# Kernel optimization log

Hardware: AMD Instinct MI355X
Metric: run time of the kernel (lower is better)

## Reference

```python
import jax, jax.numpy as jnp
import numpy as np
from jax import lax

B, N, C = 8, 16384, 4
NUM_GROUPS = 128
GROUP_SIZE = 32
GROUP_RADIUS = 0.1
UPSCALE_K = 128
OVERLAP_FACTOR = 0.7


def setup_inputs() -> dict:
    key = jax.random.key(0)
    k1, k2 = jax.random.split(key)
    # xyz in [0,1]^3, energy in [0,1] at channel 3
    points = jax.random.uniform(k1, (B, N, C), dtype=jnp.float32)
    lengths = jax.random.randint(k2, (B,), N // 2, N + 1).astype(jnp.int32)
    return {"points": points, "lengths": lengths}


def _fps(xyz, lengths, K):
    """Farthest point sampling. xyz: (B,N,3) -> centers (B,K,3), idx (B,K)."""
    B_, N_, _ = xyz.shape
    valid = jnp.arange(N_)[None, :] < lengths[:, None]          # (B,N)
    mind0 = jnp.where(valid, jnp.inf, -jnp.inf)                 # running min dist
    start = jnp.zeros((B_,), jnp.int32)                         # fixed start point
    batch = jnp.arange(B_)

    def step(carry, _):
        mind, cur = carry
        c = xyz[batch, cur]                                     # (B,3)
        d = jnp.sum((xyz - c[:, None, :]) ** 2, axis=-1)        # (B,N)
        mind = jnp.minimum(mind, jnp.where(valid, d, -jnp.inf))
        nxt = jnp.argmax(mind, axis=1).astype(jnp.int32)
        return (mind, nxt), cur

    _, idxs = lax.scan(step, (mind0, start), None, length=K)
    idxs = idxs.T                                               # (B,K)
    centers = xyz[batch[:, None], idxs]                         # (B,K,3)
    return centers, idxs


def _cnms(centers, radius, overlap_factor):
    """Greedy cluster-NMS over FPS-ordered centers. Returns keep mask (B,G)."""
    B_, G, _ = centers.shape
    d2 = jnp.sum((centers[:, :, None, :] - centers[:, None, :, :]) ** 2, axis=-1)
    thr = (2.0 * radius * (1.0 - overlap_factor)) ** 2          # spheres overlap > factor

    def step(keep, j):
        conflict = jnp.any(keep & (d2[:, j, :] < thr), axis=-1)
        keep = keep.at[:, j].set(~conflict)
        return keep, None

    keep, _ = lax.scan(step, jnp.zeros((B_, G), bool), jnp.arange(G))
    return keep


def _ball_query(centers, xyz, lengths, retain, K, radius):
    """First-K points within radius of each center (pytorch3d semantics); -1 pad."""
    N_ = xyz.shape[1]
    d2 = jnp.sum((centers[:, :, None, :] - xyz[:, None, :, :]) ** 2, axis=-1)  # (B,G,N)
    in_len = (jnp.arange(N_)[None, :] < lengths[:, None])[:, None, :]
    valid = (d2 <= radius * radius) & in_len & retain[:, :, None]
    # pick the K smallest point indices among valid ones -> "first K found"
    key_ = jnp.where(valid, jnp.arange(N_, dtype=jnp.int32)[None, None, :], N_)
    negv, _ = lax.top_k(-key_, K)                               # (B,G,K)
    idx = -negv
    return jnp.where(idx == N_, -1, idx)


def reference(points, lengths):
    xyz = points[..., :3]
    centers, _ = _fps(xyz, lengths, NUM_GROUPS)                 # (B,G,3)
    retain = _cnms(centers, GROUP_RADIUS, OVERLAP_FACTOR)       # (B,G)
    idx = _ball_query(centers, xyz, lengths, retain, UPSCALE_K, GROUP_RADIUS)

    # select_topk_by_energy (energies_idx = 3)
    batch = jnp.arange(points.shape[0])[:, None, None]
    invalid = idx == -1
    energies = jnp.where(invalid, -jnp.inf, points[batch, jnp.clip(idx, 0), 3])
    topv, topi = lax.top_k(energies, GROUP_SIZE)                # (B,G,K_new)
    tidx = jnp.take_along_axis(idx, topi, axis=2)
    tidx = jnp.where(jnp.isneginf(topv), -1, tidx)

    # fill_empty_indices: replace -1 with the group's first index
    fidx = jnp.where(tidx == -1, tidx[:, :, :1], tidx)

    # masked_gather: -1 -> gather 0 then zero out
    groups = points[batch, jnp.clip(fidx, 0)]                   # (B,G,K,C)
    groups = jnp.where((fidx == -1)[..., None], 0.0, groups)

    group_lengths = jnp.sum(jnp.all(tidx != -1, axis=2), axis=1)  # (B,)
    embedding_mask = jnp.arange(NUM_GROUPS)[None, :] < group_lengths[:, None]

    # center xyz channels, then scale ALL channels by radius (as in source)
    groups = groups.at[..., :3].add(-centers[:, :, None, :])
    groups = groups / GROUP_RADIUS
    return groups, centers, embedding_mask
```

## Files before the change

kernel.cpp:

```cpp
#include <hip/hip_runtime.h>
#include <math.h>

#define B_ 8
#define N_ 16384
#define G_ 128
#define GS_ 32
#define UK_ 128
#define FPS_T 512
#define FPS_W 8
#define PPT 32
#define BQ_T 512
#define BQ_W 8

#pragma clang fp contract(off)

typedef float v2f __attribute__((ext_vector_type(2)));

#define DPP64_MAXSTEP(vv, ctrl, rmask)                                          \
  {                                                                             \
    unsigned _lo = (unsigned)__builtin_amdgcn_update_dpp(                       \
        0, (int)(unsigned)((vv) & 0xffffffffull), (ctrl), (rmask), 0xf, false); \
    unsigned _hi = (unsigned)__builtin_amdgcn_update_dpp(                       \
        0, (int)(unsigned)((vv) >> 32), (ctrl), (rmask), 0xf, false);           \
    unsigned long long _tv = ((unsigned long long)_hi << 32) | _lo;             \
    if (_tv > (vv)) (vv) = _tv;                                                 \
  }

__device__ __forceinline__ float dist2(float x, float y, float z,
                                       float cx, float cy, float cz) {
    float dx = __fsub_rn(x, cx);
    float dy = __fsub_rn(y, cy);
    float dz = __fsub_rn(z, cz);
    return __fadd_rn(__fadd_rn(__fmul_rn(dx, dx), __fmul_rn(dy, dy)),
                     __fmul_rn(dz, dz));
}

__global__ void init_kernel(int* __restrict__ gl) {
    int t = threadIdx.x;
    if (t < B_) gl[t] = 0;
}

__global__ __launch_bounds__(FPS_T, 2) void fps_cnms_kernel(
    const float4* __restrict__ pts, const int* __restrict__ lengths,
    float* __restrict__ centers_out, int* __restrict__ keep_out) {
    const int b = blockIdx.x;
    const int t = threadIdx.x;
    const int lane = t & 63;
    const int wv = t >> 6;
    const int len = lengths[b];
    const float4* p = pts + (size_t)b * N_;

    __shared__ __align__(16) unsigned long long s_part[2][FPS_W];
    __shared__ float s_cen[G_][3];

    v2f xp[PPT / 2], yp[PPT / 2], zp[PPT / 2];
    v2f mp[PPT / 2];
#pragma unroll
    for (int j = 0; j < PPT / 2; j += 2) {
        int nA0 = (2 * j) * FPS_T + t;
        float4 qA0, qB0, qA1, qB1;
        const float4* a0 = p + nA0;
        const float4* b0 = a0 + FPS_T;
        const float4* a1 = a0 + 2 * FPS_T;
        const float4* b1 = a0 + 3 * FPS_T;
        asm volatile(
            "global_load_dwordx4 %0, %4, off\n\t"
            "global_load_dwordx4 %1, %5, off\n\t"
            "global_load_dwordx4 %2, %6, off\n\t"
            "global_load_dwordx4 %3, %7, off\n\t"
            "s_waitcnt vmcnt(0)"
            : "=&v"(qA0), "=&v"(qB0), "=&v"(qA1), "=&v"(qB1)
            : "v"(a0), "v"(b0), "v"(a1), "v"(b1)
            : "memory");
        xp[j]     = (v2f){qA0.x, qB0.x};
        yp[j]     = (v2f){qA0.y, qB0.y};
        zp[j]     = (v2f){qA0.z, qB0.z};
        xp[j + 1] = (v2f){qA1.x, qB1.x};
        yp[j + 1] = (v2f){qA1.y, qB1.y};
        zp[j + 1] = (v2f){qA1.z, qB1.z};
        v2f mm0, mm1;
        mm0.x = (nA0 < len)             ? INFINITY : -INFINITY;
        mm0.y = (nA0 + FPS_T < len)     ? INFINITY : -INFINITY;
        mm1.x = (nA0 + 2 * FPS_T < len) ? INFINITY : -INFINITY;
        mm1.y = (nA0 + 3 * FPS_T < len) ? INFINITY : -INFINITY;
        mp[j] = mm0;
        mp[j + 1] = mm1;
    }

    int n = 0;
    for (int k = 0; k < G_; k++) {
        float4 c = p[n];
        if (t == 0) {
            centers_out[(b * G_ + k) * 3 + 0] = c.x;
            centers_out[(b * G_ + k) * 3 + 1] = c.y;
            centers_out[(b * G_ + k) * 3 + 2] = c.z;
            s_cen[k][0] = c.x; s_cen[k][1] = c.y; s_cen[k][2] = c.z;
        }
        if (k == G_ - 1) break;

        v2f cXX = {c.x, c.x};
        v2f cYY = {c.y, c.y};
        v2f cZZ = {c.z, c.z};

#pragma unroll
        for (int j = 0; j < PPT / 2; j++) {
            v2f dx = xp[j] - cXX;
            v2f dy = yp[j] - cYY;
            v2f dz = zp[j] - cZZ;
            v2f dd = (dx * dx + dy * dy) + dz * dz;
            mp[j] = __builtin_elementwise_min(mp[j], dd);
        }

        v2f t8[8];
#pragma unroll
        for (int j = 0; j < 8; j++)
            t8[j] = __builtin_elementwise_max(mp[2 * j], mp[2 * j + 1]);
        v2f t4a = __builtin_elementwise_max(t8[0], t8[1]);
        v2f t4b = __builtin_elementwise_max(t8[2], t8[3]);
        v2f t4c = __builtin_elementwise_max(t8[4], t8[5]);
        v2f t4d = __builtin_elementwise_max(t8[6], t8[7]);
        v2f t2a = __builtin_elementwise_max(t4a, t4b);
        v2f t2b = __builtin_elementwise_max(t4c, t4d);
        v2f t1 = __builtin_elementwise_max(t2a, t2b);
        float bv = fmaxf(t1.x, t1.y);

        int bi = 0;
#pragma unroll
        for (int j = PPT / 2 - 1; j >= 0; j--) {
            bool hx = (mp[j].x == bv);
            bool hy = (mp[j].y == bv);
            int cand = 2 * j + (hx ? 0 : 1);
            if (hx || hy) bi = cand;
        }

        unsigned u = __float_as_uint(bv);
        u = (u & 0x80000000u) ? ~u : (u | 0x80000000u);
        int bn = (bi << 9) | t;
        unsigned long long v = ((unsigned long long)u << 32) | (unsigned)(~bn);

        DPP64_MAXSTEP(v, 0x111, 0xf);
        DPP64_MAXSTEP(v, 0x112, 0xf);
        DPP64_MAXSTEP(v, 0x114, 0xf);
        DPP64_MAXSTEP(v, 0x118, 0xf);
        DPP64_MAXSTEP(v, 0x142, 0xa);
        DPP64_MAXSTEP(v, 0x143, 0xc);
        if (lane == 63) s_part[k & 1][wv] = v;
        __syncthreads();

        unsigned long long m = s_part[k & 1][lane & 7];
        DPP64_MAXSTEP(m, 0x111, 0xf);
        DPP64_MAXSTEP(m, 0x112, 0xf);
        DPP64_MAXSTEP(m, 0x114, 0xf);
        unsigned wlo = (unsigned)__builtin_amdgcn_readlane(
            (int)(unsigned)(m & 0xffffffffull), 7);
        n = (int)(~wlo);
    }

    __syncthreads();

    if (t < 64) {
        const float THR = (float)((2.0 * 0.1 * (1.0 - 0.7)) * (2.0 * 0.1 * (1.0 - 0.7)));
        float ax = s_cen[t][0],      ay = s_cen[t][1],      az = s_cen[t][2];
        float ex = s_cen[t + 64][0], ey = s_cen[t + 64][1], ez = s_cen[t + 64][2];
        bool k0 = false, k1 = false;
        for (int j = 0; j < G_; j++) {
            float jx = s_cen[j][0], jy = s_cen[j][1], jz = s_cen[j][2];
            bool c0 = k0 && (dist2(ax, ay, az, jx, jy, jz) < THR);
            bool c1 = k1 && (dist2(ex, ey, ez, jx, jy, jz) < THR);
            bool conflict = __any(c0 || c1);
            if (j == t)      k0 = !conflict;
            if (j == t + 64) k1 = !conflict;
        }
        keep_out[b * G_ + t]      = k0 ? 1 : 0;
        keep_out[b * G_ + t + 64] = k1 ? 1 : 0;
    }
}

__global__ __launch_bounds__(BQ_T) void group_kernel(
    const float4* __restrict__ pts, const int* __restrict__ lengths,
    const float* __restrict__ centers, const int* __restrict__ keep,
    float* __restrict__ groups_out, int* __restrict__ gl) {
    const int bid = blockIdx.x;
    const int b = bid >> 7;
    const int t = threadIdx.x;
    const int lane = t & 63;
    const int wv = t >> 6;

    const float cx = centers[bid * 3 + 0];
    const float cy = centers[bid * 3 + 1];
    const float cz = centers[bid * 3 + 2];
    float4* out4 = (float4*)(groups_out + (size_t)bid * GS_ * 4);

    if (!keep[bid]) {
        if (t < GS_) {
            float4 o;
            o.x = __fdiv_rn(__fsub_rn(0.f, cx), 0.1f);
            o.y = __fdiv_rn(__fsub_rn(0.f, cy), 0.1f);
            o.z = __fdiv_rn(__fsub_rn(0.f, cz), 0.1f);
            o.w = 0.f;
            out4[t] = o;
        }
        return;
    }

    __shared__ int   s_widx[BQ_W][UK_];
    __shared__ float s_wen[BQ_W][UK_];
    __shared__ int   s_wcnt[BQ_W];
    __shared__ int   s_list[UK_];
    __shared__ float s_en[UK_];
    __shared__ int   s_ord[GS_];

    const int len = lengths[b];
    const float R2 = (float)(0.1 * 0.1);
    const float4* p = pts + (size_t)b * N_;

    {
        const int base0 = wv * (N_ / BQ_W);
        int cnt = 0;
        for (int it = 0; it < (N_ / BQ_W) / 64; it++) {
            int n = base0 + it * 64 + lane;
            float4 q = p[n];
            float d2 = dist2(q.x, q.y, q.z, cx, cy, cz);
            bool pred = (n < len) && (d2 <= R2);
            unsigned long long m = __ballot(pred);
            int prefix = __popcll(m & ((1ull << lane) - 1ull));
            int slot = cnt + prefix;
            if (pred && slot < UK_) { s_widx[wv][slot] = n; s_wen[wv][slot] = q.w; }
            cnt += __popcll(m);
        }
        if (lane == 0) s_wcnt[wv] = (cnt < UK_) ? cnt : UK_;
    }
    __syncthreads();

    int M = 0;
#pragma unroll
    for (int w = 0; w < BQ_W; w++) M += s_wcnt[w];
    if (M > UK_) M = UK_;

    if (t < UK_ && t < M) {
        int j = t, w = 0;
        while (w < BQ_W - 1 && j >= s_wcnt[w]) { j -= s_wcnt[w]; w++; }
        s_list[t] = s_widx[w][j];
        s_en[t]   = s_wen[w][j];
    }
    __syncthreads();

    if (wv == 0) {
        float v0 = (lane < M) ? s_en[lane] : -INFINITY;
        float v1 = (lane + 64 < M) ? s_en[lane + 64] : -INFINITY;
        for (int k = 0; k < GS_; k++) {
            float bv; int bs;
            if (v0 >= v1) { bv = v0; bs = lane; }
            else          { bv = v1; bs = lane + 64; }
#pragma unroll
            for (int off = 32; off; off >>= 1) {
                float ov = __shfl_xor(bv, off);
                int   os = __shfl_xor(bs, off);
                bool tk = (ov > bv) || (ov == bv && os < bs);
                bv = tk ? ov : bv; bs = tk ? os : bs;
            }
            if (lane == 0) s_ord[k] = (bv == -INFINITY) ? -1 : bs;
            if (bs == lane)           v0 = -INFINITY;
            else if (bs == lane + 64) v1 = -INFINITY;
        }
    }
    __syncthreads();

    if (t < GS_) {
        int o0 = s_ord[0];
        int first = (o0 >= 0) ? s_list[o0] : -1;
        int ok = s_ord[t];
        int ti = (ok >= 0) ? s_list[ok] : -1;
        int f = (ti == -1) ? first : ti;
        float px = 0.f, py = 0.f, pz = 0.f, pw = 0.f;
        if (f >= 0) { float4 q = p[f]; px = q.x; py = q.y; pz = q.z; pw = q.w; }
        float4 o;
        o.x = __fdiv_rn(__fsub_rn(px, cx), 0.1f);
        o.y = __fdiv_rn(__fsub_rn(py, cy), 0.1f);
        o.z = __fdiv_rn(__fsub_rn(pz, cz), 0.1f);
        o.w = __fdiv_rn(pw, 0.1f);
        out4[t] = o;
    }
    if (t == 0 && M >= GS_) atomicAdd(&gl[b], 1);
}

__global__ void mask_kernel(const int* __restrict__ gl, float* __restrict__ mask_out) {
    int t = threadIdx.x;
    int b = t >> 7, g = t & 127;
    mask_out[t] = (g < gl[b]) ? 1.0f : 0.0f;
}

extern "C" void kernel_launch(void* const* d_in, const int* in_sizes, int n_in,
                              void* d_out, int out_size, void* d_ws, size_t ws_size,
                              hipStream_t stream) {
    const float4* pts = (const float4*)d_in[0];
    const int* lengths = (const int*)d_in[1];
    float* out = (float*)d_out;
    float* groups = out;
    float* centers = out + (size_t)B_ * G_ * GS_ * 4;
    float* mask = centers + (size_t)B_ * G_ * 3;
    int* keep = (int*)d_ws;
    int* gl = keep + B_ * G_;

    hipLaunchKernelGGL(init_kernel, dim3(1), dim3(64), 0, stream, gl);
    hipLaunchKernelGGL(fps_cnms_kernel, dim3(B_), dim3(FPS_T), 0, stream,
                       pts, lengths, centers, keep);
    hipLaunchKernelGGL(group_kernel, dim3(B_ * G_), dim3(BQ_T), 0, stream,
                       pts, lengths, centers, keep, groups, gl);
    hipLaunchKernelGGL(mask_kernel, dim3(1), dim3(B_ * G_), 0, stream, gl, mask);
}
```

Before: 324.0 us.

## Split FPS across four cooperating blocks per batch with global-memory argmax exchange

Each batch's farthest point sampling is now spread over four workgroups, each holding one quarter of the points in registers. Each step's per-block argmax is published to a global slot array and merged by spinning on the other blocks' relaxed atomic loads. This cuts per-thread work and register pressure on the serial FPS critical path, which previously used only eight blocks. The cost is a cross-block global-memory handshake every iteration, and the spin-waits assume all 32 blocks are co-resident; otherwise the kernel could deadlock.

```diff
diff --git a/kernel.cpp b/kernel.cpp
--- a/kernel.cpp
+++ b/kernel.cpp
@@ -8,7 +8,9 @@
 #define UK_ 128
 #define FPS_T 512
 #define FPS_W 8
-#define PPT 32
+#define FPS_BLK 4
+#define SLICE (N_ / FPS_BLK)
+#define PPT (SLICE / FPS_T)
 #define BQ_T 512
 #define BQ_W 8
 
@@ -26,6 +28,17 @@
     if (_tv > (vv)) (vv) = _tv;                                                 \
   }
 
+__device__ __forceinline__ unsigned long long shfl_xor_u64(unsigned long long v, int m) {
+    int lo = __shfl_xor((int)(unsigned)(v & 0xffffffffull), m);
+    int hi = __shfl_xor((int)(unsigned)(v >> 32), m);
+    return ((unsigned long long)(unsigned)hi << 32) | (unsigned)lo;
+}
+
+__device__ __forceinline__ unsigned long long umax64(unsigned long long a,
+                                                     unsigned long long b) {
+    return a > b ? a : b;
+}
+
 __device__ __forceinline__ float dist2(float x, float y, float z,
                                        float cx, float cy, float cz) {
     float dx = __fsub_rn(x, cx);
@@ -35,20 +48,27 @@
                      __fmul_rn(dz, dz));
 }
 
-__global__ void init_kernel(int* __restrict__ gl) {
+__global__ void init_kernel(unsigned long long* __restrict__ slots,
+                            int* __restrict__ gl) {
     int t = threadIdx.x;
+#pragma unroll
+    for (int i = 0; i < (B_ * G_ * FPS_BLK) / 1024; i++)
+        slots[i * 1024 + t] = 0ull;
     if (t < B_) gl[t] = 0;
 }
 
 __global__ __launch_bounds__(FPS_T, 2) void fps_cnms_kernel(
     const float4* __restrict__ pts, const int* __restrict__ lengths,
-    float* __restrict__ centers_out, int* __restrict__ keep_out) {
-    const int b = blockIdx.x;
+    float* __restrict__ centers_out, int* __restrict__ keep_out,
+    unsigned long long* __restrict__ slots) {
+    const int b = blockIdx.x & 7;
+    const int slice = blockIdx.x >> 3;
     const int t = threadIdx.x;
     const int lane = t & 63;
     const int wv = t >> 6;
     const int len = lengths[b];
     const float4* p = pts + (size_t)b * N_;
+    const int base = slice * SLICE;
 
     __shared__ __align__(16) unsigned long long s_part[2][FPS_W];
     __shared__ float s_cen[G_][3];
@@ -57,7 +77,7 @@
     v2f mp[PPT / 2];
 #pragma unroll
     for (int j = 0; j < PPT / 2; j += 2) {
-        int nA0 = (2 * j) * FPS_T + t;
+        int nA0 = base + (2 * j) * FPS_T + t;
         float4 qA0, qB0, qA1, qB1;
         const float4* a0 = p + nA0;
         const float4* b0 = a0 + FPS_T;
@@ -90,7 +110,7 @@
     int n = 0;
     for (int k = 0; k < G_; k++) {
         float4 c = p[n];
-        if (t == 0) {
+        if (slice == 0 && t == 0) {
             centers_out[(b * G_ + k) * 3 + 0] = c.x;
             centers_out[(b * G_ + k) * 3 + 1] = c.y;
             centers_out[(b * G_ + k) * 3 + 2] = c.z;
@@ -111,17 +131,9 @@
             mp[j] = __builtin_elementwise_min(mp[j], dd);
         }
 
-        v2f t8[8];
-#pragma unroll
-        for (int j = 0; j < 8; j++)
-            t8[j] = __builtin_elementwise_max(mp[2 * j], mp[2 * j + 1]);
-        v2f t4a = __builtin_elementwise_max(t8[0], t8[1]);
-        v2f t4b = __builtin_elementwise_max(t8[2], t8[3]);
-        v2f t4c = __builtin_elementwise_max(t8[4], t8[5]);
-        v2f t4d = __builtin_elementwise_max(t8[6], t8[7]);
-        v2f t2a = __builtin_elementwise_max(t4a, t4b);
-        v2f t2b = __builtin_elementwise_max(t4c, t4d);
-        v2f t1 = __builtin_elementwise_max(t2a, t2b);
+        v2f t2a = __builtin_elementwise_max(mp[0], mp[1]);
+        v2f t2b = __builtin_elementwise_max(mp[2], mp[3]);
+        v2f t1  = __builtin_elementwise_max(t2a, t2b);
         float bv = fmaxf(t1.x, t1.y);
 
         int bi = 0;
@@ -135,7 +147,7 @@
 
         unsigned u = __float_as_uint(bv);
         u = (u & 0x80000000u) ? ~u : (u | 0x80000000u);
-        int bn = (bi << 9) | t;
+        int bn = base | (bi << 9) | t;
         unsigned long long v = ((unsigned long long)u << 32) | (unsigned)(~bn);
 
         DPP64_MAXSTEP(v, 0x111, 0xf);
@@ -151,14 +163,33 @@
         DPP64_MAXSTEP(m, 0x111, 0xf);
         DPP64_MAXSTEP(m, 0x112, 0xf);
         DPP64_MAXSTEP(m, 0x114, 0xf);
-        unsigned wlo = (unsigned)__builtin_amdgcn_readlane(
+        unsigned klo = (unsigned)__builtin_amdgcn_readlane(
             (int)(unsigned)(m & 0xffffffffull), 7);
+        unsigned khi = (unsigned)__builtin_amdgcn_readlane(
+            (int)(unsigned)(m >> 32), 7);
+        unsigned long long kk = ((unsigned long long)khi << 32) | klo;
+
+        unsigned long long* slot = slots + ((size_t)b * G_ + k) * FPS_BLK;
+        if (wv == 0 && lane == 0)
+            __hip_atomic_store(&slot[slice], kk, __ATOMIC_RELAXED,
+                               __HIP_MEMORY_SCOPE_AGENT);
+        unsigned long long pv = kk;
+        if (lane < FPS_BLK && lane != slice) {
+            do {
+                pv = __hip_atomic_load(&slot[lane], __ATOMIC_RELAXED,
+                                       __HIP_MEMORY_SCOPE_AGENT);
+            } while (pv == 0ull);
+        }
+        unsigned long long mg = umax64(pv, shfl_xor_u64(pv, 1));
+        mg = umax64(mg, shfl_xor_u64(mg, 2));
+        unsigned wlo = (unsigned)__builtin_amdgcn_readfirstlane(
+            (int)(unsigned)(mg & 0xffffffffull));
         n = (int)(~wlo);
     }
 
     __syncthreads();
 
-    if (t < 64) {
+    if (slice == 0 && t < 64) {
         const float THR = (float)((2.0 * 0.1 * (1.0 - 0.7)) * (2.0 * 0.1 * (1.0 - 0.7)));
         float ax = s_cen[t][0],      ay = s_cen[t][1],      az = s_cen[t][2];
         float ex = s_cen[t + 64][0], ey = s_cen[t + 64][1], ez = s_cen[t + 64][2];
@@ -299,12 +330,13 @@
     float* groups = out;
     float* centers = out + (size_t)B_ * G_ * GS_ * 4;
     float* mask = centers + (size_t)B_ * G_ * 3;
-    int* keep = (int*)d_ws;
+    unsigned long long* slots = (unsigned long long*)d_ws;
+    int* keep = (int*)(slots + B_ * G_ * FPS_BLK);
     int* gl = keep + B_ * G_;
 
-    hipLaunchKernelGGL(init_kernel, dim3(1), dim3(64), 0, stream, gl);
-    hipLaunchKernelGGL(fps_cnms_kernel, dim3(B_), dim3(FPS_T), 0, stream,
-                       pts, lengths, centers, keep);
+    hipLaunchKernelGGL(init_kernel, dim3(1), dim3(1024), 0, stream, slots, gl);
+    hipLaunchKernelGGL(fps_cnms_kernel, dim3(B_ * FPS_BLK), dim3(FPS_T), 0, stream,
+                       pts, lengths, centers, keep, slots);
     hipLaunchKernelGGL(group_kernel, dim3(B_ * G_), dim3(BQ_T), 0, stream,
                        pts, lengths, centers, keep, groups, gl);
     hipLaunchKernelGGL(mask_kernel, dim3(1), dim3(B_ * G_), 0, stream, gl, mask);
```

After: 292.0 us. -9.9%, faster.
